# Kernel optimization log

Hardware: AMD Instinct MI355X
Metric: run time of the kernel (lower is better)

The kernel has to match this reference:

```python
import jax, jax.numpy as jnp
import numpy as np


def setup_inputs() -> dict:
    key = jax.random.key(0)
    k1, k2, k3 = jax.random.split(key, 3)
    x = jax.random.normal(k1, (1, 512, 14, 14), dtype=jnp.float32)
    w1 = jax.random.normal(k2, (16, 64, 3), dtype=jnp.float32)
    w2 = jax.random.normal(k3, (32, 8, 3), dtype=jnp.float32)
    return {"x": x, "w1": w1, "w2": w2}


def reference(x, w1, w2):
    SHIFT = 1  # module picks +/-1 at random init; fixed to +1
    H = W = 14
    # reshape (1,512,14,14) -> (1, i=64, o=8, H, W), roll along H
    xr = x.reshape(1, 64, 8, H, W)
    xr = jnp.roll(xr, SHIFT, axis=3)
    # unfold with kernel (3,1), pad (1,0) along H == stack 3 shifted slices
    xp = jnp.pad(xr, ((0, 0), (0, 0), (0, 0), (1, 1), (0, 0)))
    t3 = jnp.stack([xp[:, :, :, j:j + H, :] for j in range(3)], axis=3)  # (1,64,8,3,14,14)
    # conv 1: contract i=64 channels and j=3 taps per group o -> k=16 outputs
    t4 = jnp.einsum('liojmn,kij->lkomn', t3, w1)  # (1,16,8,14,14)
    # unfold with kernel (3,1), pad (1,0) along W (after the (1,1792,14,1) reshape)
    tp = jnp.pad(t4, ((0, 0), (0, 0), (0, 0), (0, 0), (1, 1)))
    t5 = jnp.stack([tp[..., k:k + W] for k in range(3)], axis=4)  # (1,16,8,14,3,14)
    # conv 2: contract j=8 group channels and k=3 taps -> i=32 outputs per o=16
    t6 = jnp.einsum('lojmkn,ijk->liomn', t5, w2)  # (1,32,16,14,14)
    return t6.reshape(1, 512, H, W)
```

## Files before the change

kernel.cpp:

```cpp
#include <hip/hip_runtime.h>


__global__ __launch_bounds__(128) void fused_shift_conv(
    const float* __restrict__ x,
    const float* __restrict__ w1,
    const float* __restrict__ w2,
    float* __restrict__ out)
{
    const int bx = blockIdx.x;
    const int m  = bx >> 4;
    const int o2 = bx & 15;
    const int t  = threadIdx.x;

    __shared__ float w1s[64 * 3];
    __shared__ float w2s[32 * 8 * 3];
    __shared__ float t4s[8 * 14];

    for (int idx = t; idx < 192; idx += 128) w1s[idx] = w1[o2 * 192 + idx];
    for (int idx = t; idx < 768; idx += 128) w2s[idx] = w2[idx];
    __syncthreads();

    if (t < 112) {
        const int o = t / 14;
        const int n = t % 14;
        float acc = 0.f;
        #pragma unroll
        for (int j = 0; j < 3; ++j) {
            const int hp = m + j - 1;
            if (hp < 0 || hp >= 14) continue;
            const int row = (hp + 13) % 14;
            const float* xp = x + (size_t)o * 196 + row * 14 + n;
            const float* wp = w1s + j;
            #pragma unroll
            for (int i = 0; i < 64; ++i) {
                acc += xp[(size_t)i * 8 * 196] * wp[i * 3];
            }
        }
        t4s[t] = acc;
    }
    __syncthreads();

    for (int idx = t; idx < 448; idx += 128) {
        const int n  = idx % 14;
        const int i2 = idx / 14;
        const float* wp = w2s + i2 * 24;
        float acc = 0.f;
        #pragma unroll
        for (int j = 0; j < 8; ++j) {
            const float* tp = t4s + j * 14;
            #pragma unroll
            for (int k = 0; k < 3; ++k) {
                const int nn = n + k - 1;
                if (nn >= 0 && nn < 14) acc += tp[nn] * wp[j * 3 + k];
            }
        }
        out[((size_t)(i2 * 16 + o2) * 14 + m) * 14 + n] = acc;
    }
}

extern "C" void kernel_launch(void* const* d_in, const int* in_sizes, int n_in,
                              void* d_out, int out_size, void* d_ws, size_t ws_size,
                              hipStream_t stream) {
    const float* x  = (const float*)d_in[0];
    const float* w1 = (const float*)d_in[1];
    const float* w2 = (const float*)d_in[2];
    float* out = (float*)d_out;
    fused_shift_conv<<<dim3(224), dim3(128), 0, stream>>>(x, w1, w2, out);
}
```

Baseline: 66.82 us.

## Split conv1 channel reduction across four thread groups with 512-thread blocks

Raises the block size from 128 to 512 threads. The 64-channel reduction of the first conv is split into four 16-channel partial sums, which are combined in shared memory through an extra barrier. The second conv now uses one thread per output with no loop, and w2 is loaded with float4. This shortens the serial dependent-load chain per thread and adds memory-level parallelism, at the cost of an extra sync and more threads per block.

```diff
diff --git a/kernel.cpp b/kernel.cpp
--- a/kernel.cpp
+++ b/kernel.cpp
@@ -1,7 +1,7 @@
 #include <hip/hip_runtime.h>
 
 
-__global__ __launch_bounds__(128) void fused_shift_conv(
+__global__ __launch_bounds__(512) void fused_shift_conv(
     const float* __restrict__ x,
     const float* __restrict__ w1,
     const float* __restrict__ w2,
@@ -14,35 +14,44 @@
 
     __shared__ float w1s[64 * 3];
     __shared__ float w2s[32 * 8 * 3];
-    __shared__ float t4s[8 * 14];
+    __shared__ float t4p[4][112];
+    __shared__ float t4s[112];
 
-    for (int idx = t; idx < 192; idx += 128) w1s[idx] = w1[o2 * 192 + idx];
-    for (int idx = t; idx < 768; idx += 128) w2s[idx] = w2[idx];
+    if (t < 192) w1s[t] = w1[o2 * 192 + t];
+    if (t >= 256 && t < 256 + 192) {
+        ((float4*)w2s)[t - 256] = ((const float4*)w2)[t - 256];
+    }
     __syncthreads();
 
-    if (t < 112) {
-        const int o = t / 14;
-        const int n = t % 14;
+    if (t < 448) {
+        const int quarter = t / 112;
+        const int r = t % 112;
+        const int o = r / 14;
+        const int n = r % 14;
+        const int ibase = quarter * 16;
         float acc = 0.f;
         #pragma unroll
         for (int j = 0; j < 3; ++j) {
             const int hp = m + j - 1;
-            if (hp < 0 || hp >= 14) continue;
-            const int row = (hp + 13) % 14;
-            const float* xp = x + (size_t)o * 196 + row * 14 + n;
-            const float* wp = w1s + j;
-            #pragma unroll
-            for (int i = 0; i < 64; ++i) {
-                acc += xp[(size_t)i * 8 * 196] * wp[i * 3];
+            if (hp >= 0 && hp < 14) {
+                const int row = (hp + 13) % 14;
+                const float* xp = x + (size_t)(ibase * 8 + o) * 196 + row * 14 + n;
+                const float* wp = w1s + ibase * 3 + j;
+                #pragma unroll
+                for (int i = 0; i < 16; ++i) {
+                    acc += xp[(size_t)i * 8 * 196] * wp[i * 3];
+                }
             }
         }
-        t4s[t] = acc;
+        t4p[quarter][r] = acc;
     }
     __syncthreads();
+    if (t < 112) t4s[t] = (t4p[0][t] + t4p[1][t]) + (t4p[2][t] + t4p[3][t]);
+    __syncthreads();
 
-    for (int idx = t; idx < 448; idx += 128) {
-        const int n  = idx % 14;
-        const int i2 = idx / 14;
+    if (t < 448) {
+        const int n  = t % 14;
+        const int i2 = t / 14;
         const float* wp = w2s + i2 * 24;
         float acc = 0.f;
         #pragma unroll
@@ -65,5 +74,5 @@
     const float* w1 = (const float*)d_in[1];
     const float* w2 = (const float*)d_in[2];
     float* out = (float*)d_out;
-    fused_shift_conv<<<dim3(224), dim3(128), 0, stream>>>(x, w1, w2, out);
+    fused_shift_conv<<<dim3(224), dim3(512), 0, stream>>>(x, w1, w2, out);
 }
```

Result: faster. 59.99 us (-10.2%).
